# Optimization experiments

Hardware: AMD Instinct MI355X
Metric: run time of the kernel (lower is better)

## Reference

```python
import jax, jax.numpy as jnp
import numpy as np

B, N, M, D = 16, 4096, 4096, 3


def setup_inputs() -> dict:
    key = jax.random.key(0)
    k1, k2 = jax.random.split(key)
    xyz1 = jax.random.normal(k1, (B, N, D), dtype=jnp.float32)
    xyz2 = jax.random.normal(k2, (B, M, D), dtype=jnp.float32)
    return {"xyz1": xyz1, "xyz2": xyz2}


def _chamfer(xyz1, xyz2):
    # Squared pairwise distances via ||a||^2 + ||b||^2 - 2 a.b  -> [B, N, M]
    s1 = jnp.sum(xyz1 * xyz1, axis=-1)                     # [B, N]
    s2 = jnp.sum(xyz2 * xyz2, axis=-1)                     # [B, M]
    cross = jnp.einsum("bnd,bmd->bnm", xyz1, xyz2)        # [B, N, M]
    d2 = s1[:, :, None] + s2[:, None, :] - 2.0 * cross
    d2 = jnp.maximum(d2, 0.0)  # guard tiny negatives from cancellation
    dist1 = jnp.min(d2, axis=2)  # nearest point in set2 for each point in set1, [B, N]
    dist2 = jnp.min(d2, axis=1)  # nearest point in set1 for each point in set2, [B, M]
    return dist1, dist2


def reference(xyz1, xyz2):
    return _chamfer(xyz1, xyz2)
```

## Files before the change

### kernel.cpp

```cpp
#include <hip/hip_runtime.h>

typedef _Float16 h8     __attribute__((ext_vector_type(8)));
typedef float    f32x16 __attribute__((ext_vector_type(16)));

#define BB      16
#define NPTS    4096
#define WAVES   4
#define RPW     64
#define RPB     (WAVES * RPW)
#define CHUNK   512
#define NCHUNK  (NPTS / CHUNK)
#define TPB     (WAVES * 64)

__global__ __launch_bounds__(TPB) void chamfer_mfma(
    const float* __restrict__ xyz1,
    const float* __restrict__ xyz2,
    float* __restrict__ out)
{
    __shared__ __align__(16) _Float16 sb[2][CHUNK * 16];

    const int tid  = threadIdx.x;
    const int lane = tid & 63;
    const int wv   = tid >> 6;
    const int rb   = blockIdx.x;
    const int b    = blockIdx.y;
    const int dir  = blockIdx.z;

    const float* qbase = (dir == 0 ? xyz1 : xyz2) + b * NPTS * 3;
    const float* dbase = (dir == 0 ? xyz2 : xyz1) + b * NPTS * 3;

    h8 af[2];
#pragma unroll
    for (int rbi = 0; rbi < 2; ++rbi) {
        const int row = rb * RPB + wv * RPW + rbi * 32 + (lane & 31);
        float x = qbase[row * 3 + 0], y = qbase[row * 3 + 1], z = qbase[row * 3 + 2];
        float s = fmaf(x, x, fmaf(y, y, z * z));
        _Float16 xh = (_Float16)x, yh = (_Float16)y, zh = (_Float16)z;
        _Float16 xl = (_Float16)(x - (float)xh);
        _Float16 yl = (_Float16)(y - (float)yh);
        _Float16 zl = (_Float16)(z - (float)zh);
        _Float16 sh = (_Float16)s;
        _Float16 sl = (_Float16)(s - (float)sh);
        _Float16 one = (_Float16)1.0f, zero = (_Float16)0.0f;
        af[rbi] = (lane < 32) ? h8{xh, yh, zh, xh, yh, zh, xl, yl}
                              : h8{zl, sh, sl, one, one, zero, zero, zero};
    }

    const f32x16 Z = {};
    float rm[2][16];
#pragma unroll
    for (int rbi = 0; rbi < 2; ++rbi)
#pragma unroll
        for (int r = 0; r < 16; ++r) rm[rbi][r] = 3.0e38f;

    const int loff = ((lane >> 5) << 8) + (lane & 31) * 8;

    float v[4][3];

    auto stage_load = [&](int ch) {
        const float* p = dbase + ch * CHUNK * 3;
#pragma unroll
        for (int t = 0; t < 4; ++t) {
            int c = (tid + t * TPB) >> 1;
            v[t][0] = p[c * 3 + 0];
            v[t][1] = p[c * 3 + 1];
            v[t][2] = p[c * 3 + 2];
        }
    };
    auto stage_write = [&](int buf) {
#pragma unroll
        for (int t = 0; t < 4; ++t) {
            int it = tid + t * TPB;
            int c = it >> 1, hf = it & 1;
            float x = v[t][0], y = v[t][1], z = v[t][2];
            float s = fmaf(x, x, fmaf(y, y, z * z));
            _Float16 xh = (_Float16)x, yh = (_Float16)y, zh = (_Float16)z;
            _Float16 m2xh = (_Float16)(-2.0f) * xh;
            _Float16 m2yh = (_Float16)(-2.0f) * yh;
            _Float16 m2zh = (_Float16)(-2.0f) * zh;
            _Float16 m2xl = (_Float16)(-2.0f * (x - (float)xh));
            _Float16 m2yl = (_Float16)(-2.0f * (y - (float)yh));
            _Float16 m2zl = (_Float16)(-2.0f * (z - (float)zh));
            _Float16 sh = (_Float16)s;
            _Float16 sl = (_Float16)(s - (float)sh);
            _Float16 one = (_Float16)1.0f, zero = (_Float16)0.0f;
            h8 w = (hf == 0) ? h8{m2xh, m2yh, m2zh, m2xl, m2yl, m2zl, m2xh, m2yh}
                             : h8{m2zh, one, one, sh, sl, zero, zero, zero};
            int off = (c >> 5) * 512 + (hf << 8) + (c & 31) * 8;
            *(h8*)&sb[buf][off] = w;
        }
    };

    auto sweep = [&](int buf) {
        const _Float16* base = &sb[buf][0];
#pragma unroll 2
        for (int t = 0; t < CHUNK / 32; t += 2) {
            h8 b0 = *(const h8*)(base + t * 512 + loff);
            h8 b1 = *(const h8*)(base + (t + 1) * 512 + loff);
#pragma unroll
            for (int rbi = 0; rbi < 2; ++rbi) {
                f32x16 a0 = __builtin_amdgcn_mfma_f32_32x32x16_f16(af[rbi], b0, Z, 0, 0, 0);
                f32x16 a1 = __builtin_amdgcn_mfma_f32_32x32x16_f16(af[rbi], b1, Z, 0, 0, 0);
#pragma unroll
                for (int r = 0; r < 16; ++r)
                    rm[rbi][r] = fminf(fminf(a0[r], a1[r]), rm[rbi][r]);
            }
        }
    };

    stage_load(0);
    stage_write(0);
    __syncthreads();
#pragma unroll 1
    for (int ch = 0; ch < NCHUNK; ++ch) {
        int buf = ch & 1;
        if (ch + 1 < NCHUNK) stage_load(ch + 1);
        sweep(buf);
        if (ch + 1 < NCHUNK) stage_write(buf ^ 1);
        __syncthreads();
    }

#pragma unroll
    for (int rbi = 0; rbi < 2; ++rbi)
#pragma unroll
        for (int r = 0; r < 16; ++r) {
            float m = rm[rbi][r];
            m = fminf(m, __shfl_xor(m, 1));
            m = fminf(m, __shfl_xor(m, 2));
            m = fminf(m, __shfl_xor(m, 4));
            m = fminf(m, __shfl_xor(m, 8));
            m = fminf(m, __shfl_xor(m, 16));
            rm[rbi][r] = m;
        }
    if ((lane & 31) == 0) {
        const int half = lane >> 5;
        float* o = out + dir * (BB * NPTS) + b * NPTS + rb * RPB + wv * RPW;
#pragma unroll
        for (int rbi = 0; rbi < 2; ++rbi)
#pragma unroll
            for (int r = 0; r < 16; ++r) {
                int rr = (r & 3) + 8 * (r >> 2) + 4 * half;
                o[rbi * 32 + rr] = fmaxf(rm[rbi][r], 0.0f);
            }
    }
}

extern "C" void kernel_launch(void* const* d_in, const int* in_sizes, int n_in,
                              void* d_out, int out_size, void* d_ws, size_t ws_size,
                              hipStream_t stream) {
    const float* xyz1 = (const float*)d_in[0];
    const float* xyz2 = (const float*)d_in[1];
    float* out = (float*)d_out;

    dim3 grid(NPTS / RPB, BB, 2);
    hipLaunchKernelGGL(chamfer_mfma, grid, dim3(TPB), 0, stream, xyz1, xyz2, out);
}
```

Measured before the change: 37.35 us.

## Split the column range across blocks and merge minima with integer atomicMin

Splits the database points into two halves handled by separate blocks, doubling the grid from 512 to 1024 blocks for better CU occupancy. Partial minima are merged with integer atomicMin on the float bit pattern, which is valid because values are clamped non-negative. An init kernel fills the output with a large sentinel first. The staging chunk shrinks to 256 points, one point per thread, and the sweep loop is fully unrolled. Costs are an extra kernel launch and atomic traffic.

```diff
diff --git a/kernel.cpp b/kernel.cpp
--- a/kernel.cpp
+++ b/kernel.cpp
@@ -8,9 +8,16 @@
 #define WAVES   4
 #define RPW     64
 #define RPB     (WAVES * RPW)
-#define CHUNK   512
-#define NCHUNK  (NPTS / CHUNK)
+#define CSPLIT  2
+#define COLS    (NPTS / CSPLIT)
+#define CHUNK   256
+#define NCHUNK  (COLS / CHUNK)
 #define TPB     (WAVES * 64)
+
+__global__ __launch_bounds__(256) void chamfer_init_out(float* __restrict__ out) {
+    int i = blockIdx.x * 256 + threadIdx.x;
+    out[i] = 3.0e38f;
+}
 
 __global__ __launch_bounds__(TPB) void chamfer_mfma(
     const float* __restrict__ xyz1,
@@ -24,21 +31,23 @@
     const int wv   = tid >> 6;
     const int rb   = blockIdx.x;
     const int b    = blockIdx.y;
-    const int dir  = blockIdx.z;
+    const int z    = blockIdx.z;
+    const int dir  = z & 1;
+    const int csp  = z >> 1;
 
     const float* qbase = (dir == 0 ? xyz1 : xyz2) + b * NPTS * 3;
-    const float* dbase = (dir == 0 ? xyz2 : xyz1) + b * NPTS * 3;
+    const float* dbase = (dir == 0 ? xyz2 : xyz1) + b * NPTS * 3 + csp * COLS * 3;
 
     h8 af[2];
 #pragma unroll
     for (int rbi = 0; rbi < 2; ++rbi) {
         const int row = rb * RPB + wv * RPW + rbi * 32 + (lane & 31);
-        float x = qbase[row * 3 + 0], y = qbase[row * 3 + 1], z = qbase[row * 3 + 2];
-        float s = fmaf(x, x, fmaf(y, y, z * z));
-        _Float16 xh = (_Float16)x, yh = (_Float16)y, zh = (_Float16)z;
+        float x = qbase[row * 3 + 0], y = qbase[row * 3 + 1], z2 = qbase[row * 3 + 2];
+        float s = fmaf(x, x, fmaf(y, y, z2 * z2));
+        _Float16 xh = (_Float16)x, yh = (_Float16)y, zh = (_Float16)z2;
         _Float16 xl = (_Float16)(x - (float)xh);
         _Float16 yl = (_Float16)(y - (float)yh);
-        _Float16 zl = (_Float16)(z - (float)zh);
+        _Float16 zl = (_Float16)(z2 - (float)zh);
         _Float16 sh = (_Float16)s;
         _Float16 sl = (_Float16)(s - (float)sh);
         _Float16 one = (_Float16)1.0f, zero = (_Float16)0.0f;
@@ -55,45 +64,31 @@
 
     const int loff = ((lane >> 5) << 8) + (lane & 31) * 8;
 
-    float v[4][3];
-
+    float vx, vy, vz;
     auto stage_load = [&](int ch) {
-        const float* p = dbase + ch * CHUNK * 3;
-#pragma unroll
-        for (int t = 0; t < 4; ++t) {
-            int c = (tid + t * TPB) >> 1;
-            v[t][0] = p[c * 3 + 0];
-            v[t][1] = p[c * 3 + 1];
-            v[t][2] = p[c * 3 + 2];
-        }
+        const float* p = dbase + (ch * CHUNK + tid) * 3;
+        vx = p[0]; vy = p[1]; vz = p[2];
     };
     auto stage_write = [&](int buf) {
-#pragma unroll
-        for (int t = 0; t < 4; ++t) {
-            int it = tid + t * TPB;
-            int c = it >> 1, hf = it & 1;
-            float x = v[t][0], y = v[t][1], z = v[t][2];
-            float s = fmaf(x, x, fmaf(y, y, z * z));
-            _Float16 xh = (_Float16)x, yh = (_Float16)y, zh = (_Float16)z;
-            _Float16 m2xh = (_Float16)(-2.0f) * xh;
-            _Float16 m2yh = (_Float16)(-2.0f) * yh;
-            _Float16 m2zh = (_Float16)(-2.0f) * zh;
-            _Float16 m2xl = (_Float16)(-2.0f * (x - (float)xh));
-            _Float16 m2yl = (_Float16)(-2.0f * (y - (float)yh));
-            _Float16 m2zl = (_Float16)(-2.0f * (z - (float)zh));
-            _Float16 sh = (_Float16)s;
-            _Float16 sl = (_Float16)(s - (float)sh);
-            _Float16 one = (_Float16)1.0f, zero = (_Float16)0.0f;
-            h8 w = (hf == 0) ? h8{m2xh, m2yh, m2zh, m2xl, m2yl, m2zl, m2xh, m2yh}
-                             : h8{m2zh, one, one, sh, sl, zero, zero, zero};
-            int off = (c >> 5) * 512 + (hf << 8) + (c & 31) * 8;
-            *(h8*)&sb[buf][off] = w;
-        }
+        float s = fmaf(vx, vx, fmaf(vy, vy, vz * vz));
+        _Float16 xh = (_Float16)vx, yh = (_Float16)vy, zh = (_Float16)vz;
+        _Float16 m2xh = (_Float16)(-2.0f) * xh;
+        _Float16 m2yh = (_Float16)(-2.0f) * yh;
+        _Float16 m2zh = (_Float16)(-2.0f) * zh;
+        _Float16 m2xl = (_Float16)(-2.0f * (vx - (float)xh));
+        _Float16 m2yl = (_Float16)(-2.0f * (vy - (float)yh));
+        _Float16 m2zl = (_Float16)(-2.0f * (vz - (float)zh));
+        _Float16 sh = (_Float16)s;
+        _Float16 sl = (_Float16)(s - (float)sh);
+        _Float16 one = (_Float16)1.0f, zero = (_Float16)0.0f;
+        int off = (tid >> 5) * 512 + (tid & 31) * 8;
+        *(h8*)&sb[buf][off]       = h8{m2xh, m2yh, m2zh, m2xl, m2yl, m2zl, m2xh, m2yh};
+        *(h8*)&sb[buf][off + 256] = h8{m2zh, one, one, sh, sl, zero, zero, zero};
     };
 
     auto sweep = [&](int buf) {
         const _Float16* base = &sb[buf][0];
-#pragma unroll 2
+#pragma unroll
         for (int t = 0; t < CHUNK / 32; t += 2) {
             h8 b0 = *(const h8*)(base + t * 512 + loff);
             h8 b1 = *(const h8*)(base + (t + 1) * 512 + loff);
@@ -134,13 +129,14 @@
         }
     if ((lane & 31) == 0) {
         const int half = lane >> 5;
-        float* o = out + dir * (BB * NPTS) + b * NPTS + rb * RPB + wv * RPW;
+        int* o = (int*)out + dir * (BB * NPTS) + b * NPTS + rb * RPB + wv * RPW;
 #pragma unroll
         for (int rbi = 0; rbi < 2; ++rbi)
 #pragma unroll
             for (int r = 0; r < 16; ++r) {
                 int rr = (r & 3) + 8 * (r >> 2) + 4 * half;
-                o[rbi * 32 + rr] = fmaxf(rm[rbi][r], 0.0f);
+                float val = fmaxf(rm[rbi][r], 0.0f);
+                atomicMin(o + rbi * 32 + rr, __float_as_int(val));
             }
     }
 }
@@ -152,6 +148,8 @@
     const float* xyz2 = (const float*)d_in[1];
     float* out = (float*)d_out;
 
-    dim3 grid(NPTS / RPB, BB, 2);
+    hipLaunchKernelGGL(chamfer_init_out, dim3(2 * BB * NPTS / 256), dim3(256), 0, stream, out);
+
+    dim3 grid(NPTS / RPB, BB, 2 * CSPLIT);
     hipLaunchKernelGGL(chamfer_mfma, grid, dim3(TPB), 0, stream, xyz1, xyz2, out);
 }
```

Measured after the change: 71.65 us. 1.92x slower.
